# Performance work log

Hardware: AMD Instinct MI355X
Metric: run time of the kernel (lower is better)

Reference implementation:

```python
import jax, jax.numpy as jnp
import numpy as np
from jax import lax

N, D, H, E = 8192, 1024, 4096, 8


def setup_inputs() -> dict:
    key = jax.random.key(0)
    ks = jax.random.split(key, 4)
    return {
        "x": jax.random.normal(ks[0], (N, D), dtype=jnp.float32),
        "wg": jax.random.normal(ks[1], (D, E), dtype=jnp.float32) * 0.001,
        "fc1_w": jax.random.normal(ks[2], (E, D, H), dtype=jnp.float32) * 0.001,
        "fc1_b": jnp.zeros((E, 1, H), dtype=jnp.float32),
        "fc2_w": jax.random.normal(ks[3], (E, H, D), dtype=jnp.float32) * 0.001,
        "fc2_b": jnp.zeros((E, 1, D), dtype=jnp.float32),
        "k": 2,
    }


def reference(x, wg, fc1_w, fc1_b, fc2_w, fc2_b, k):
    n, d = x.shape
    e = wg.shape[1]
    cap = (k * n) // e  # expert capacity (capacity factor 1.0)

    # --- gate ---
    scores = jax.nn.softmax(x @ wg, axis=-1)          # [N,E]
    topv, topi = lax.top_k(scores, k)                 # [N,k]

    # --- top-k routing: position of each (token, slot) within its expert buffer ---
    masks = jax.nn.one_hot(topi, e, dtype=jnp.int32)  # [N,k,E]
    # slot-major priority: all slot-0 assignments before slot-1
    m = jnp.transpose(masks, (1, 0, 2)).reshape(k * n, e)
    pos_flat = jnp.cumsum(m, axis=0) - m              # position before own assignment
    pos = jnp.sum(pos_flat * m, axis=1).reshape(k, n).T   # [N,k]
    valid = pos < cap                                  # capacity overflow -> dropped

    # --- load-balance aux loss (top-1 fraction * mean gate prob) ---
    me = scores.mean(axis=0)                           # [E]
    ce = masks[:, 0, :].astype(scores.dtype).mean(axis=0)
    l_aux = e * jnp.sum(me * ce)

    # --- encode (dispatch): scatter tokens into [E, C, D] buffers ---
    w = valid.astype(x.dtype)                          # [N,k]
    flat_idx = topi * cap + jnp.where(valid, pos, 0)   # [N,k]
    contrib = (x[:, None, :] * w[:, :, None]).reshape(-1, d)
    dispatched = jnp.zeros((e * cap, d), x.dtype).at[flat_idx.reshape(-1)].add(contrib)
    dispatched = dispatched.reshape(e, cap, d)

    # --- batched expert FFN (all-to-all is identity on one device) ---
    h = jax.nn.relu(jnp.einsum('ecd,edh->ech', dispatched, fc1_w) + fc1_b)
    y = jnp.einsum('ech,ehd->ecd', h, fc2_w) + fc2_b   # [E,C,D]

    # --- decode (combine): gather back and weight by gate scores ---
    gathered = y.reshape(e * cap, d)[flat_idx]         # [N,k,D]
    output = jnp.einsum('nk,nkd->nd', topv * w, gathered)
    return output, l_aux
```

## Files before the change

kernel.cpp:

```cpp
#include <hip/hip_runtime.h>
#include <hip/hip_bf16.h>
#include <stdint.h>

#define N_TOK 8192
#define DMODEL 1024
#define HDIM 4096
#define NEXP 8
#define CAP 2048
#define GATE_BLOCKS (N_TOK / 4)

typedef float floatx4 __attribute__((ext_vector_type(4)));
typedef int int32x4_t __attribute__((ext_vector_type(4)));
typedef int int32x8_t __attribute__((ext_vector_type(8)));

static __device__ __forceinline__ void async_copy16(const void* g, void* l) {
  __builtin_amdgcn_global_load_lds(
      (const __attribute__((address_space(1))) void*)g,
      (__attribute__((address_space(3))) void*)l, 16, 0, 0);
}

static __device__ __forceinline__ unsigned int pk4_fp8(float a, float b, float c, float d) {
  int r = __builtin_amdgcn_cvt_pk_fp8_f32(a, b, 0, 0);
  r = __builtin_amdgcn_cvt_pk_fp8_f32(c, d, r, 1);
  return (unsigned int)r;
}

static __device__ __forceinline__ unsigned short f2bf(float f) {
  union { float f; uint32_t u; } v; v.f = f;
  uint32_t r = (v.u + 0x7FFFu + ((v.u >> 16) & 1u)) >> 16;
  return (unsigned short)r;
}

static __device__ __forceinline__ float bf2f(unsigned short u) {
  union { float f; uint32_t u32; } v; v.u32 = ((uint32_t)u) << 16;
  return v.f;
}

__global__ __launch_bounds__(256) void gate_transpose_kernel(
    const float* __restrict__ fc1_w, unsigned char* __restrict__ fc1t,
    const float* __restrict__ fc2_w, unsigned char* __restrict__ fc2t,
    const float* __restrict__ x, const float* __restrict__ wg,
    float* __restrict__ topv, int* __restrict__ topi,
    float* __restrict__ me_part, int* __restrict__ ce_part) {
  __shared__ float tile[32][129];
  __shared__ float sm_p[4][NEXP];
  __shared__ int sm_i0[4];
  int z = blockIdx.z;
  if (z < 16) {
    const float* in; unsigned char* out; int R, C, bx, by, zz;
    if (z < 8) {
      in = fc1_w; out = fc1t; R = DMODEL; C = HDIM; zz = z;
      bx = blockIdx.x; by = blockIdx.y;
    } else {
      in = fc2_w; out = fc2t; R = HDIM; C = DMODEL; zz = z - 8;
      bx = blockIdx.x & 31; by = blockIdx.y * 4 + (blockIdx.x >> 5);
    }
    const float* inp = in + (size_t)zz * R * C;
    unsigned char* outp = out + (size_t)zz * R * C;
    int c0 = bx * 32, r0 = by * 128;
    int t = threadIdx.x;
#pragma unroll
    for (int p = 0; p < 4; p++) {
      int r = p * 32 + (t >> 3);
      int c4 = (t & 7) * 4;
      float4 v = *(const float4*)(inp + (size_t)(r0 + r) * C + c0 + c4);
      tile[c4 + 0][r] = v.x; tile[c4 + 1][r] = v.y;
      tile[c4 + 2][r] = v.z; tile[c4 + 3][r] = v.w;
    }
    __syncthreads();
    int c = t >> 3, r16 = (t & 7) * 16;
    unsigned int w[4];
#pragma unroll
    for (int j = 0; j < 4; j++) {
      float a = tile[c][r16 + j * 4 + 0] * 512.f;
      float b = tile[c][r16 + j * 4 + 1] * 512.f;
      float cc2 = tile[c][r16 + j * 4 + 2] * 512.f;
      float d = tile[c][r16 + j * 4 + 3] * 512.f;
      w[j] = pk4_fp8(a, b, cc2, d);
    }
    uint4 o; o.x = w[0]; o.y = w[1]; o.z = w[2]; o.w = w[3];
    *(uint4*)(outp + (size_t)(c0 + c) * R + r0 + r16) = o;
    return;
  }
  int gb = (z - 16) * 1024 + blockIdx.y * 128 + blockIdx.x;
  int wave = threadIdx.x >> 6;
  int lane = threadIdx.x & 63;
  int n = gb * 4 + wave;
  float acc[NEXP];
#pragma unroll
  for (int e = 0; e < NEXP; e++) acc[e] = 0.f;
  const float* xr = x + (size_t)n * DMODEL;
#pragma unroll 4
  for (int i = 0; i < DMODEL / 64; i++) {
    int idx = lane + 64 * i;
    float xv = xr[idx];
    const float4* wr = (const float4*)(wg + (size_t)idx * NEXP);
    float4 w0 = wr[0], w1 = wr[1];
    acc[0] += xv * w0.x; acc[1] += xv * w0.y;
    acc[2] += xv * w0.z; acc[3] += xv * w0.w;
    acc[4] += xv * w1.x; acc[5] += xv * w1.y;
    acc[6] += xv * w1.z; acc[7] += xv * w1.w;
  }
#pragma unroll
  for (int e = 0; e < NEXP; e++) {
    float v = acc[e];
#pragma unroll
    for (int off = 32; off > 0; off >>= 1) v += __shfl_down(v, off, 64);
    acc[e] = v;
  }
  if (lane == 0) {
    float mx = acc[0];
#pragma unroll
    for (int e = 1; e < NEXP; e++) mx = fmaxf(mx, acc[e]);
    float p[NEXP]; float s = 0.f;
#pragma unroll
    for (int e = 0; e < NEXP; e++) { p[e] = expf(acc[e] - mx); s += p[e]; }
    float inv = 1.f / s;
#pragma unroll
    for (int e = 0; e < NEXP; e++) p[e] *= inv;
    int i0 = 0; float v0 = p[0];
#pragma unroll
    for (int e = 1; e < NEXP; e++) if (p[e] > v0) { v0 = p[e]; i0 = e; }
    int i1 = -1; float v1 = -1.f;
#pragma unroll
    for (int e = 0; e < NEXP; e++) {
      if (e == i0) continue;
      if (p[e] > v1) { v1 = p[e]; i1 = e; }
    }
    topv[n * 2] = v0; topv[n * 2 + 1] = v1;
    topi[n * 2] = i0; topi[n * 2 + 1] = i1;
#pragma unroll
    for (int e = 0; e < NEXP; e++) sm_p[wave][e] = p[e];
    sm_i0[wave] = i0;
  }
  __syncthreads();
  if (threadIdx.x < NEXP) {
    int e = threadIdx.x;
    float pm = 0.f; int cc = 0;
#pragma unroll
    for (int w = 0; w < 4; w++) {
      pm += sm_p[w][e];
      cc += (sm_i0[w] == e) ? 1 : 0;
    }
    me_part[gb * NEXP + e] = pm;
    ce_part[gb * NEXP + e] = cc;
  }
}

__global__ __launch_bounds__(1024) void scan_kernel(
    const int* __restrict__ topi, const float* __restrict__ topv,
    int* __restrict__ flat_idx, float* __restrict__ cw,
    const float* __restrict__ me_part, const int* __restrict__ ce_part,
    float* __restrict__ out_laux) {
  __shared__ int hist[16][NEXP];
  __shared__ int base[NEXP];
  __shared__ float redm[NEXP][2];
  __shared__ float redc[NEXP][2];
  int tid = threadIdx.x;
  int w = tid >> 6, lane = tid & 63;
  if (tid < NEXP) base[tid] = 0;
  int vals[16];
#pragma unroll
  for (int c = 0; c < 16; c++) {
    int j = c * 1024 + tid;
    vals[c] = topi[(size_t)(j & 8191) * 2 + (j >> 13)];
  }
  __syncthreads();
  for (int c = 0; c < 16; c++) {
    int j = c * 1024 + tid;
    int slot = j >> 13;
    int n = j & 8191;
    int e = vals[c];
    int rank = 0;
#pragma unroll
    for (int ee = 0; ee < NEXP; ee++) {
      unsigned long long m = __ballot(e == ee);
      if (e == ee) rank = __popcll(m & ((1ull << lane) - 1ull));
      if (lane == ee) hist[w][ee] = __popcll(m);
    }
    __syncthreads();
    if (tid < NEXP) {
      int run = base[tid];
#pragma unroll
      for (int ww = 0; ww < 16; ww++) {
        int t = hist[ww][tid];
        hist[ww][tid] = run;
        run += t;
      }
      base[tid] = run;
    }
    __syncthreads();
    int pos = hist[w][e] + rank;
    bool valid = pos < CAP;
    flat_idx[n * 2 + slot] = e * CAP + (valid ? pos : 0);
    cw[n * 2 + slot] = valid ? topv[n * 2 + slot] : 0.f;
    __syncthreads();
  }
  {
    int e2 = tid >> 7, c2 = tid & 127;
    float pm = 0.f, cc = 0.f;
    for (int b = c2; b < GATE_BLOCKS; b += 128) {
      pm += me_part[b * NEXP + e2];
      cc += (float)ce_part[b * NEXP + e2];
    }
#pragma unroll
    for (int off = 32; off > 0; off >>= 1) {
      pm += __shfl_down(pm, off, 64);
      cc += __shfl_down(cc, off, 64);
    }
    if ((tid & 63) == 0) {
      redm[e2][(tid >> 6) & 1] = pm;
      redc[e2][(tid >> 6) & 1] = cc;
    }
    __syncthreads();
    if (tid == 0) {
      float s = 0.f;
#pragma unroll
      for (int ee = 0; ee < NEXP; ee++) {
        float tm2 = redm[ee][0] + redm[ee][1];
        float tc2 = redc[ee][0] + redc[ee][1];
        s += (tm2 / (float)N_TOK) * (tc2 / (float)N_TOK);
      }
      *out_laux = (float)NEXP * s;
    }
  }
}

__global__ __launch_bounds__(64) void dispatch_kernel(
    const float* __restrict__ x, const int* __restrict__ flat_idx,
    const float* __restrict__ cw, unsigned char* __restrict__ disp) {
  int a = blockIdx.x;
  if (cw[a] == 0.f) return;
  int n = a >> 1;
  int f = flat_idx[a];
  int lane = threadIdx.x;
  const float4* xr = (const float4*)(x + (size_t)n * DMODEL);
  unsigned int* dr = (unsigned int*)(disp + (size_t)f * DMODEL);
#pragma unroll
  for (int i = 0; i < 4; i++) {
    float4 v = xr[lane + 64 * i];
    dr[lane + 64 * i] = pk4_fp8(v.x, v.y, v.z, v.w);
  }
}

template <int K_DIM, bool RELU, int OUT_MODE>
__global__ __launch_bounds__(256) void gemm_fp8_kernel(
    const unsigned char* __restrict__ A, const unsigned char* __restrict__ BT,
    const float* __restrict__ bias, void* __restrict__ Cout, int M, int Ncols,
    float inv_scale, float out_mult) {
  constexpr int BK = 128;
  constexpr int NSTAGE = K_DIM / BK;
  static_assert(NSTAGE >= 2, "need >=2 K stages for the 2-deep pipeline");
  __shared__ unsigned char As[2][128 * BK];
  __shared__ unsigned char Bs[2][128 * BK];

  unsigned gx = gridDim.x;
  unsigned gxy = gridDim.x * gridDim.y;
  unsigned nwg = gxy * gridDim.z;
  unsigned lid = blockIdx.z * gxy + blockIdx.y * gx + blockIdx.x;
  int e, tm, tn;
  if ((nwg & 7u) == 0u) {
    unsigned chunk = nwg >> 3;
    unsigned w = (lid & 7u) * chunk + (lid >> 3);
    e = w / gxy;
    unsigned rem = w - (unsigned)e * gxy;
    tm = rem / gx;
    tn = rem - (unsigned)tm * gx;
  } else {
    e = blockIdx.z; tm = blockIdx.y; tn = blockIdx.x;
  }

  const unsigned char* Ae = A + (size_t)e * M * K_DIM + (size_t)tm * 128 * K_DIM;
  const unsigned char* Be = BT + (size_t)e * Ncols * K_DIM + (size_t)tn * 128 * K_DIM;
  int wv = threadIdx.x >> 6, l = threadIdx.x & 63;
  int wm = wv >> 1, wn = wv & 1;
  int l15 = l & 15, quad = l >> 4;
  int rbase = wv * 8 + (l >> 3);
  int cg = (l & 7) ^ ((l >> 3) & 7);
  floatx4 acc[4][4] = {};

#define STAGE_LOADS(k0, buf)                                                   \
  {                                                                            \
    _Pragma("unroll") for (int i = 0; i < 4; i++) {                            \
      int r = rbase + i * 32;                                                  \
      async_copy16(Ae + (size_t)r * K_DIM + (k0) + cg * 16,                    \
                   &As[buf][i * 4096 + wv * 1024]);                            \
      async_copy16(Be + (size_t)r * K_DIM + (k0) + cg * 16,                    \
                   &Bs[buf][i * 4096 + wv * 1024]);                            \
    }                                                                          \
  }

#define READ_AF(mi)                                                            \
  {                                                                            \
    int m = wm * 64 + (mi) * 16 + l15;                                         \
    int x0 = (quad * 2) ^ (m & 7), x1 = (quad * 2 + 1) ^ (m & 7);              \
    int32x4_t lo = *(const int32x4_t*)(&As[cur][m * 128 + x0 * 16]);           \
    int32x4_t hi = *(const int32x4_t*)(&As[cur][m * 128 + x1 * 16]);           \
    af[mi] = __builtin_shufflevector(lo, hi, 0, 1, 2, 3, 4, 5, 6, 7);          \
  }

  STAGE_LOADS(0, 0);
  STAGE_LOADS(BK, 1);
#pragma unroll
  for (int s = 0; s < NSTAGE; s++) {
    const int cur = s & 1;
    if (s + 1 < NSTAGE)
      asm volatile("s_waitcnt vmcnt(8)" ::: "memory");
    else
      asm volatile("s_waitcnt vmcnt(0)" ::: "memory");
    __builtin_amdgcn_s_barrier();
    int32x8_t af[4], bf[4];
#pragma unroll
    for (int ni = 0; ni < 4; ni++) {
      int m = wn * 64 + ni * 16 + l15;
      int x0 = (quad * 2) ^ (m & 7), x1 = (quad * 2 + 1) ^ (m & 7);
      int32x4_t lo = *(const int32x4_t*)(&Bs[cur][m * 128 + x0 * 16]);
      int32x4_t hi = *(const int32x4_t*)(&Bs[cur][m * 128 + x1 * 16]);
      bf[ni] = __builtin_shufflevector(lo, hi, 0, 1, 2, 3, 4, 5, 6, 7);
    }
    READ_AF(0);
    __builtin_amdgcn_sched_barrier(0);
    READ_AF(1);
    READ_AF(2);
    READ_AF(3);
    __builtin_amdgcn_sched_barrier(0);
    __builtin_amdgcn_s_setprio(1);
    asm volatile("s_waitcnt lgkmcnt(6)" ::: "memory");
    __builtin_amdgcn_sched_barrier(0);
#pragma unroll
    for (int ni = 0; ni < 4; ni++)
      acc[0][ni] = __builtin_amdgcn_mfma_scale_f32_16x16x128_f8f6f4(
          af[0], bf[ni], acc[0][ni], 0, 0, 0, 0x7F7F7F7F, 0, 0x7F7F7F7F);
    asm volatile("s_waitcnt lgkmcnt(4)" ::: "memory");
    __builtin_amdgcn_sched_barrier(0);
#pragma unroll
    for (int ni = 0; ni < 4; ni++)
      acc[1][ni] = __builtin_amdgcn_mfma_scale_f32_16x16x128_f8f6f4(
          af[1], bf[ni], acc[1][ni], 0, 0, 0, 0x7F7F7F7F, 0, 0x7F7F7F7F);
    asm volatile("s_waitcnt lgkmcnt(2)" ::: "memory");
    __builtin_amdgcn_sched_barrier(0);
#pragma unroll
    for (int ni = 0; ni < 4; ni++)
      acc[2][ni] = __builtin_amdgcn_mfma_scale_f32_16x16x128_f8f6f4(
          af[2], bf[ni], acc[2][ni], 0, 0, 0, 0x7F7F7F7F, 0, 0x7F7F7F7F);
    asm volatile("s_waitcnt lgkmcnt(0)" ::: "memory");
    __builtin_amdgcn_sched_barrier(0);
    __builtin_amdgcn_s_setprio(0);
    __builtin_amdgcn_s_barrier();
    if (s + 2 < NSTAGE) STAGE_LOADS((s + 2) * BK, cur);
    __builtin_amdgcn_s_setprio(1);
#pragma unroll
    for (int ni = 0; ni < 4; ni++)
      acc[3][ni] = __builtin_amdgcn_mfma_scale_f32_16x16x128_f8f6f4(
          af[3], bf[ni], acc[3][ni], 0, 0, 0, 0x7F7F7F7F, 0, 0x7F7F7F7F);
    __builtin_amdgcn_s_setprio(0);
  }
#undef STAGE_LOADS
#undef READ_AF

  int row_base = tm * 128 + wm * 64;
  int col_base = tn * 128 + wn * 64;
  const float* be = bias + (size_t)e * Ncols;
#pragma unroll
  for (int ni = 0; ni < 4; ni++) {
    int col = col_base + ni * 16 + l15;
    float bv = be[col];
#pragma unroll
    for (int mi = 0; mi < 4; mi++) {
#pragma unroll
      for (int r = 0; r < 4; r++) {
        int row = row_base + mi * 16 + quad * 4 + r;
        float v = acc[mi][ni][r] * inv_scale + bv;
        if (RELU) v = fmaxf(v, 0.f);
        size_t idx = (size_t)e * M * Ncols + (size_t)row * Ncols + col;
        if (OUT_MODE == 1) {
          float s = fminf(fmaxf(v * out_mult, -440.f), 440.f);
          unsigned int b8 = (unsigned int)__builtin_amdgcn_cvt_pk_fp8_f32(s, s, 0, 0) & 0xFF;
          ((unsigned char*)Cout)[idx] = (unsigned char)b8;
        } else if (OUT_MODE == 2) {
          ((unsigned short*)Cout)[idx] = f2bf(v);
        } else {
          ((float*)Cout)[idx] = v;
        }
      }
    }
  }
}

__global__ __launch_bounds__(256) void combine_kernel(
    const unsigned short* __restrict__ y, const int* __restrict__ flat_idx,
    const float* __restrict__ cw, float* __restrict__ out) {
  int n = blockIdx.x;
  float w0 = cw[n * 2], w1 = cw[n * 2 + 1];
  int f0 = flat_idx[n * 2], f1 = flat_idx[n * 2 + 1];
  const ushort2* y0 = (const ushort2*)(y + (size_t)f0 * DMODEL);
  const ushort2* y1 = (const ushort2*)(y + (size_t)f1 * DMODEL);
  float2* o = (float2*)(out + (size_t)n * DMODEL);
  int t = threadIdx.x;
#pragma unroll
  for (int i = 0; i < 2; i++) {
    int j = t + i * 256;
    ushort2 a = y0[j], b = y1[j];
    float2 r;
    r.x = w0 * bf2f(a.x) + w1 * bf2f(b.x);
    r.y = w0 * bf2f(a.y) + w1 * bf2f(b.y);
    o[j] = r;
  }
}

extern "C" void kernel_launch(void* const* d_in, const int* in_sizes, int n_in,
                              void* d_out, int out_size, void* d_ws,
                              size_t ws_size, hipStream_t stream) {
  (void)in_sizes; (void)n_in; (void)out_size; (void)ws_size;
  const float* x     = (const float*)d_in[0];
  const float* wg    = (const float*)d_in[1];
  const float* fc1_w = (const float*)d_in[2];
  const float* fc1_b = (const float*)d_in[3];
  const float* fc2_w = (const float*)d_in[4];
  const float* fc2_b = (const float*)d_in[5];
  float* out = (float*)d_out;

  char* ws = (char*)d_ws;
  size_t o = 0;
  unsigned char* fc1t = (unsigned char*)(ws + o); o += (size_t)NEXP * DMODEL * HDIM;
  unsigned char* fc2t = (unsigned char*)(ws + o); o += (size_t)NEXP * DMODEL * HDIM;
  unsigned char* disp = (unsigned char*)(ws + o); o += (size_t)NEXP * CAP * DMODEL;
  unsigned char* hbuf = (unsigned char*)(ws + o); o += (size_t)NEXP * CAP * HDIM;
  unsigned short* ybuf = (unsigned short*)(ws + o); o += (size_t)NEXP * CAP * DMODEL * 2;
  float* topv = (float*)(ws + o); o += (size_t)N_TOK * 2 * 4;
  int* topi   = (int*)(ws + o);   o += (size_t)N_TOK * 2 * 4;
  int* flat   = (int*)(ws + o);   o += (size_t)N_TOK * 2 * 4;
  float* cw   = (float*)(ws + o); o += (size_t)N_TOK * 2 * 4;
  float* mep  = (float*)(ws + o); o += (size_t)GATE_BLOCKS * NEXP * 4;
  int* cep    = (int*)(ws + o);   o += (size_t)GATE_BLOCKS * NEXP * 4;


  gate_transpose_kernel<<<dim3(128, 8, 18), 256, 0, stream>>>(
      fc1_w, fc1t, fc2_w, fc2t, x, wg, topv, topi, mep, cep);
  scan_kernel<<<1, 1024, 0, stream>>>(topi, topv, flat, cw, mep, cep,
                                      out + (size_t)N_TOK * DMODEL);
  dispatch_kernel<<<N_TOK * 2, 64, 0, stream>>>(x, flat, cw, disp);
  gemm_fp8_kernel<DMODEL, true, 1>
      <<<dim3(HDIM / 128, CAP / 128, NEXP), 256, 0, stream>>>(
          disp, fc1t, fc1_b, hbuf, CAP, HDIM, 1.f / 512.f, 16.f);
  gemm_fp8_kernel<HDIM, false, 2>
      <<<dim3(DMODEL / 128, CAP / 128, NEXP), 256, 0, stream>>>(
          hbuf, fc2t, fc2_b, ybuf, CAP, DMODEL, 1.f / 8192.f, 1.f);
  combine_kernel<<<N_TOK, 256, 0, stream>>>(ybuf, flat, cw, out);
}
```

Before: 550.4 us.

## Transpose weights in fp8 via byte-permute with larger 256x256 tiles

Rewrites the weight transpose+fp8 conversion so each block handles a 256x256 tile. Rows are converted to fp8 in registers first, then 4x4 byte blocks are transposed with v_perm, so the LDS staging holds packed bytes instead of floats. This cuts LDS traffic and conversion work in the transpose, and gives wider coalesced 16-byte stores along rows. The launch grid becomes 2D with fewer, larger blocks, which uses more LDS per block and may reduce occupancy.

Result: no change. 544.4 us (-1.1%).

```diff
diff --git a/kernel.cpp b/kernel.cpp
--- a/kernel.cpp
+++ b/kernel.cpp
@@ -42,49 +42,67 @@
     const float* __restrict__ x, const float* __restrict__ wg,
     float* __restrict__ topv, int* __restrict__ topi,
     float* __restrict__ me_part, int* __restrict__ ce_part) {
-  __shared__ float tile[32][129];
+  __shared__ unsigned int ldsT[256 * 65];
   __shared__ float sm_p[4][NEXP];
   __shared__ int sm_i0[4];
-  int z = blockIdx.z;
-  if (z < 16) {
-    const float* in; unsigned char* out; int R, C, bx, by, zz;
-    if (z < 8) {
-      in = fc1_w; out = fc1t; R = DMODEL; C = HDIM; zz = z;
-      bx = blockIdx.x; by = blockIdx.y;
+  int y = blockIdx.y;
+  int t = threadIdx.x;
+  int w = t >> 6, l = t & 63;
+  if (y < 16) {
+    const float* in; unsigned char* out; int R, C, r0, c0, zz;
+    int tt = blockIdx.x;
+    if (y < 8) {
+      in = fc1_w; out = fc1t; R = DMODEL; C = HDIM; zz = y;
+      r0 = (tt & 3) * 256;
+      c0 = (tt >> 2) * 256;
     } else {
-      in = fc2_w; out = fc2t; R = HDIM; C = DMODEL; zz = z - 8;
-      bx = blockIdx.x & 31; by = blockIdx.y * 4 + (blockIdx.x >> 5);
-    }
-    const float* inp = in + (size_t)zz * R * C;
-    unsigned char* outp = out + (size_t)zz * R * C;
-    int c0 = bx * 32, r0 = by * 128;
-    int t = threadIdx.x;
-#pragma unroll
-    for (int p = 0; p < 4; p++) {
-      int r = p * 32 + (t >> 3);
-      int c4 = (t & 7) * 4;
-      float4 v = *(const float4*)(inp + (size_t)(r0 + r) * C + c0 + c4);
-      tile[c4 + 0][r] = v.x; tile[c4 + 1][r] = v.y;
-      tile[c4 + 2][r] = v.z; tile[c4 + 3][r] = v.w;
+      in = fc2_w; out = fc2t; R = HDIM; C = DMODEL; zz = y - 8;
+      r0 = (tt >> 2) * 256;
+      c0 = (tt & 3) * 256;
+    }
+    const float* inp = in + (size_t)zz * R * C + c0;
+    unsigned char* outp = out + (size_t)zz * R * C + r0;
+#pragma unroll 4
+    for (int g = 0; g < 16; g++) {
+      int rr = 64 * w + 4 * g;
+      float4 v0 = *(const float4*)(inp + (size_t)(r0 + rr + 0) * C + 4 * l);
+      float4 v1 = *(const float4*)(inp + (size_t)(r0 + rr + 1) * C + 4 * l);
+      float4 v2 = *(const float4*)(inp + (size_t)(r0 + rr + 2) * C + 4 * l);
+      float4 v3 = *(const float4*)(inp + (size_t)(r0 + rr + 3) * C + 4 * l);
+      unsigned D0 = pk4_fp8(v0.x * 512.f, v0.y * 512.f, v0.z * 512.f, v0.w * 512.f);
+      unsigned D1 = pk4_fp8(v1.x * 512.f, v1.y * 512.f, v1.z * 512.f, v1.w * 512.f);
+      unsigned D2 = pk4_fp8(v2.x * 512.f, v2.y * 512.f, v2.z * 512.f, v2.w * 512.f);
+      unsigned D3 = pk4_fp8(v3.x * 512.f, v3.y * 512.f, v3.z * 512.f, v3.w * 512.f);
+      unsigned E0 = __builtin_amdgcn_perm(D1, D0, 0x05010400u);
+      unsigned E1 = __builtin_amdgcn_perm(D1, D0, 0x07030602u);
+      unsigned F0 = __builtin_amdgcn_perm(D3, D2, 0x05010400u);
+      unsigned F1 = __builtin_amdgcn_perm(D3, D2, 0x07030602u);
+      unsigned T0 = __builtin_amdgcn_perm(F0, E0, 0x05040100u);
+      unsigned T1 = __builtin_amdgcn_perm(F0, E0, 0x07060302u);
+      unsigned T2 = __builtin_amdgcn_perm(F1, E1, 0x05040100u);
+      unsigned T3 = __builtin_amdgcn_perm(F1, E1, 0x07060302u);
+      int q = 16 * w + g;
+      ldsT[(4 * l + 0) * 65 + q] = T0;
+      ldsT[(4 * l + 1) * 65 + q] = T1;
+      ldsT[(4 * l + 2) * 65 + q] = T2;
+      ldsT[(4 * l + 3) * 65 + q] = T3;
     }
     __syncthreads();
-    int c = t >> 3, r16 = (t & 7) * 16;
-    unsigned int w[4];
-#pragma unroll
-    for (int j = 0; j < 4; j++) {
-      float a = tile[c][r16 + j * 4 + 0] * 512.f;
-      float b = tile[c][r16 + j * 4 + 1] * 512.f;
-      float cc2 = tile[c][r16 + j * 4 + 2] * 512.f;
-      float d = tile[c][r16 + j * 4 + 3] * 512.f;
-      w[j] = pk4_fp8(a, b, cc2, d);
-    }
-    uint4 o; o.x = w[0]; o.y = w[1]; o.z = w[2]; o.w = w[3];
-    *(uint4*)(outp + (size_t)(c0 + c) * R + r0 + r16) = o;
+    int tr = l >> 4, tq = l & 15;
+#pragma unroll 4
+    for (int it = 0; it < 16; it++) {
+      int c = 64 * w + 4 * it + tr;
+      int base = c * 65 + 4 * tq;
+      uint4 o;
+      o.x = ldsT[base + 0]; o.y = ldsT[base + 1];
+      o.z = ldsT[base + 2]; o.w = ldsT[base + 3];
+      *(uint4*)(outp + (size_t)(c0 + c) * R + 16 * tq) = o;
+    }
     return;
   }
-  int gb = (z - 16) * 1024 + blockIdx.y * 128 + blockIdx.x;
-  int wave = threadIdx.x >> 6;
-  int lane = threadIdx.x & 63;
+  int gb = (y - 16) * 64 + blockIdx.x;
+  int wave = w;
+  int lane = l;
   int n = gb * 4 + wave;
   float acc[NEXP];
 #pragma unroll
@@ -134,13 +152,13 @@
     sm_i0[wave] = i0;
   }
   __syncthreads();
-  if (threadIdx.x < NEXP) {
-    int e = threadIdx.x;
+  if (t < NEXP) {
+    int e = t;
     float pm = 0.f; int cc = 0;
 #pragma unroll
-    for (int w = 0; w < 4; w++) {
-      pm += sm_p[w][e];
-      cc += (sm_i0[w] == e) ? 1 : 0;
+    for (int ww = 0; ww < 4; ww++) {
+      pm += sm_p[ww][e];
+      cc += (sm_i0[ww] == e) ? 1 : 0;
     }
     me_part[gb * NEXP + e] = pm;
     ce_part[gb * NEXP + e] = cc;
@@ -435,7 +453,7 @@
   int* cep    = (int*)(ws + o);   o += (size_t)GATE_BLOCKS * NEXP * 4;
 
 
-  gate_transpose_kernel<<<dim3(128, 8, 18), 256, 0, stream>>>(
+  gate_transpose_kernel<<<dim3(64, 48), 256, 0, stream>>>(
       fc1_w, fc1t, fc2_w, fc2t, x, wg, topv, topi, mep, cep);
   scan_kernel<<<1, 1024, 0, stream>>>(topi, topv, flat, cw, mep, cep,
                                       out + (size_t)N_TOK * DMODEL);
```
